# Kernel optimization log

Measured on AMD Instinct MI355X. Metric: run time of the kernel, lower is better.

Reference implementation:

```python
import jax, jax.numpy as jnp
from jax import lax
import numpy as np


def setup_inputs() -> dict:
    key = jax.random.key(0)
    ks = jax.random.split(key, 7)
    B, T, I, H, O = 8192, 512, 7, 7, 1
    s = 1.0 / np.sqrt(H)
    return {
        "x": jax.random.normal(ks[0], (B, T, I), dtype=jnp.float32),
        "W_ih": jax.random.normal(ks[1], (H, I), dtype=jnp.float32) * s,
        "W_hh": jax.random.normal(ks[2], (H, H), dtype=jnp.float32) * s,
        "b_ih": jax.random.normal(ks[3], (H,), dtype=jnp.float32) * s,
        "b_hh": jax.random.normal(ks[4], (H,), dtype=jnp.float32) * s,
        "W_fc": jax.random.normal(ks[5], (O, H), dtype=jnp.float32) * s,
        "b_fc": jax.random.normal(ks[6], (O,), dtype=jnp.float32) * s,
    }


def reference(x, W_ih, W_hh, b_ih, b_hh, W_fc, b_fc):
    # Vanilla tanh RNN: h_t = tanh(x_t W_ih^T + b_ih + h_{t-1} W_hh^T + b_hh)
    B, T, _ = x.shape
    H = W_hh.shape[0]
    # Precompute the input projection for all timesteps (one big GEMM).
    xp = jnp.einsum("bti,hi->bth", x, W_ih) + (b_ih + b_hh)  # [B,T,H]
    h0 = jnp.zeros((B, H), dtype=x.dtype)

    def step(h, xt):
        h = jnp.tanh(xt + h @ W_hh.T)
        return h, h

    hT, hs = lax.scan(step, h0, jnp.swapaxes(xp, 0, 1))  # hs: [T,B,H]
    out_seq = jnp.swapaxes(hs, 0, 1)  # [B,T,H]
    out = (jnp.einsum("bth,oh->bto", out_seq, W_fc) + b_fc).squeeze(-1)  # [B,T]
    hidden = hT[None]  # [1,B,H] matching torch's (num_layers, B, H)
    return (out, hidden)
```

## Files before the change

kernel.cpp:

```cpp
#include <hip/hip_runtime.h>
#include <stdint.h>


#define B_TOTAL 8192
#define T_STEPS 512

__device__ __forceinline__ float tanh_fast(float a) {
    float e = __builtin_amdgcn_exp2f(a * 2.8853900817779268f);
    float r = __builtin_amdgcn_rcpf(e + 1.0f);
    return __builtin_fmaf(-2.0f, r, 1.0f);
}

__global__ __launch_bounds__(256, 1) void rnn_kernel(
    const float* __restrict__ x,
    const float* __restrict__ Wih,
    const float* __restrict__ Whh,
    const float* __restrict__ bih,
    const float* __restrict__ bhh,
    const float* __restrict__ Wfc,
    const float* __restrict__ bfc,
    float* __restrict__ out)
{
    const int tid  = threadIdx.x;
    const int k    = tid & 7;
    const int b    = blockIdx.x * 32 + (tid >> 3);
    const int base = (tid & 63) & ~7;

    float wih[7], whh[7];
    float bias = 0.0f;
    if (k < 7) {
        #pragma unroll
        for (int i = 0; i < 7; ++i) {
            wih[i] = Wih[k * 7 + i];
            whh[i] = Whh[k * 7 + i];
        }
        bias = bih[k] + bhh[k];
    } else {
        #pragma unroll
        for (int i = 0; i < 7; ++i) { wih[i] = 0.0f; whh[i] = 0.0f; }
    }
    float wfc[7];
    #pragma unroll
    for (int j = 0; j < 7; ++j) wfc[j] = Wfc[j];
    const float bfcv = bfc[0];

    const float4* xrow = (const float4*)(x + (size_t)b * (T_STEPS * 7));

    float h[7];
    #pragma unroll
    for (int j = 0; j < 7; ++j) h[j] = 0.0f;

    float* outp = out + (size_t)b * T_STEPS;

    float4 bufA[14], bufB[14];
    #pragma unroll
    for (int i = 0; i < 14; ++i) bufA[i] = xrow[i];

    auto process = [&](const float4 (&buf)[14], int c) {
        float xv[56];
        #pragma unroll
        for (int i = 0; i < 14; ++i) {
            xv[4 * i + 0] = buf[i].x; xv[4 * i + 1] = buf[i].y;
            xv[4 * i + 2] = buf[i].z; xv[4 * i + 3] = buf[i].w;
        }
        float u[8];
        #pragma unroll
        for (int s = 0; s < 8; ++s) {
            float m0 = wih[0] * xv[s * 7 + 0];
            float m1 = wih[1] * xv[s * 7 + 1];
            float m2 = wih[2] * xv[s * 7 + 2];
            float m3 = wih[3] * xv[s * 7 + 3];
            float m4 = wih[4] * xv[s * 7 + 4];
            float m5 = wih[5] * xv[s * 7 + 5];
            float m6 = wih[6] * xv[s * 7 + 6];
            u[s] = ((m0 + m1) + (m2 + m3)) + ((m4 + m5) + (m6 + bias));
        }
        float o[8];
        #pragma unroll
        for (int s = 0; s < 8; ++s) {
            float r0 = whh[0] * h[0];
            float r1 = whh[1] * h[1];
            float r2 = whh[2] * h[2];
            float r3 = whh[3] * h[3];
            float r4 = whh[4] * h[4];
            float r5 = whh[5] * h[5];
            float r6 = whh[6] * h[6];
            float acc = u[s] + (((r0 + r1) + (r2 + r3)) + ((r4 + r5) + r6));
            float hk = tanh_fast(acc);
            #pragma unroll
            for (int j = 0; j < 7; ++j)
                h[j] = __shfl(hk, base + j, 64);
            float f0 = wfc[0] * h[0];
            float f1 = wfc[1] * h[1];
            float f2 = wfc[2] * h[2];
            float f3 = wfc[3] * h[3];
            float f4 = wfc[4] * h[4];
            float f5 = wfc[5] * h[5];
            float f6 = wfc[6] * h[6];
            o[s] = ((f0 + f1) + (f2 + f3)) + ((f4 + f5) + (f6 + bfcv));
        }
        if (k == 7) {
            float4 lo = make_float4(o[0], o[1], o[2], o[3]);
            float4 hi = make_float4(o[4], o[5], o[6], o[7]);
            *(float4*)(outp + c * 8 + 0) = lo;
            *(float4*)(outp + c * 8 + 4) = hi;
        }
    };

    for (int c = 0; c < 64; c += 2) {
        #pragma unroll
        for (int i = 0; i < 14; ++i) bufB[i] = xrow[(c + 1) * 14 + i];
        process(bufA, c);
        if (c + 2 < 64) {
            #pragma unroll
            for (int i = 0; i < 14; ++i) bufA[i] = xrow[(c + 2) * 14 + i];
        }
        process(bufB, c + 1);
    }

    if (k < 7) {
        out[(size_t)B_TOTAL * T_STEPS + (size_t)b * 7 + k] = h[k];
    }
}

extern "C" void kernel_launch(void* const* d_in, const int* in_sizes, int n_in,
                              void* d_out, int out_size, void* d_ws, size_t ws_size,
                              hipStream_t stream) {
    const float* x   = (const float*)d_in[0];
    const float* Wih = (const float*)d_in[1];
    const float* Whh = (const float*)d_in[2];
    const float* bih = (const float*)d_in[3];
    const float* bhh = (const float*)d_in[4];
    const float* Wfc = (const float*)d_in[5];
    const float* bfc = (const float*)d_in[6];
    float* out = (float*)d_out;

    rnn_kernel<<<dim3(B_TOTAL / 32), dim3(256), 0, stream>>>(
        x, Wih, Whh, bih, bhh, Wfc, bfc, out);
}
```

Before: 243.6 us.

## Replace LDS shuffles with DPP quad broadcasts for hidden-state exchange

Hidden-state exchange within each 8-lane group now uses DPP quad_perm broadcasts and a half-row mirror instead of seven __shfl (ds_bpermute) calls per timestep. Recurrent and output weights are pre-permuted per quad so each lane can consume its own quad's values and the mirrored values from the other quad. The dot products are also rewritten with explicit FMAs. This aims to shorten the serial per-step latency of the recurrence, at the cost of relying on exact DPP lane semantics.

```diff
diff --git a/kernel.cpp b/kernel.cpp
--- a/kernel.cpp
+++ b/kernel.cpp
@@ -4,6 +4,18 @@
 
 #define B_TOTAL 8192
 #define T_STEPS 512
+
+#define DPP_QUAD0 0x00
+#define DPP_QUAD1 0x55
+#define DPP_QUAD2 0xAA
+#define DPP_QUAD3 0xFF
+#define DPP_HALF_MIRROR 0x141
+
+template <int CTRL>
+__device__ __forceinline__ float dpp_mov(float v) {
+    int r = __builtin_amdgcn_update_dpp(0, __float_as_int(v), CTRL, 0xF, 0xF, true);
+    return __int_as_float(r);
+}
 
 __device__ __forceinline__ float tanh_fast(float a) {
     float e = __builtin_amdgcn_exp2f(a * 2.8853900817779268f);
@@ -24,33 +36,45 @@
     const int tid  = threadIdx.x;
     const int k    = tid & 7;
     const int b    = blockIdx.x * 32 + (tid >> 3);
-    const int base = (tid & 63) & ~7;
+    const int quad = (tid >> 2) & 1;
 
-    float wih[7], whh[7];
+    float wih[7];
+    float wa[4], wb[4], wfa[4], wfb[4];
     float bias = 0.0f;
-    if (k < 7) {
+    {
+        float whh_row[8];
         #pragma unroll
-        for (int i = 0; i < 7; ++i) {
-            wih[i] = Wih[k * 7 + i];
-            whh[i] = Whh[k * 7 + i];
+        for (int i = 0; i < 8; ++i) whh_row[i] = 0.0f;
+        if (k < 7) {
+            #pragma unroll
+            for (int i = 0; i < 7; ++i) {
+                wih[i] = Wih[k * 7 + i];
+                whh_row[i] = Whh[k * 7 + i];
+            }
+            bias = bih[k] + bhh[k];
+        } else {
+            #pragma unroll
+            for (int i = 0; i < 7; ++i) wih[i] = 0.0f;
         }
-        bias = bih[k] + bhh[k];
-    } else {
+        float wfc_row[8];
         #pragma unroll
-        for (int i = 0; i < 7; ++i) { wih[i] = 0.0f; whh[i] = 0.0f; }
+        for (int j = 0; j < 7; ++j) wfc_row[j] = Wfc[j];
+        wfc_row[7] = 0.0f;
+        #pragma unroll
+        for (int j = 0; j < 4; ++j) {
+            wa[j]  = quad ? whh_row[4 + j] : whh_row[j];
+            wb[j]  = quad ? whh_row[j]     : whh_row[4 + j];
+            wfa[j] = quad ? wfc_row[4 + j] : wfc_row[j];
+            wfb[j] = quad ? wfc_row[j]     : wfc_row[4 + j];
+        }
     }
-    float wfc[7];
-    #pragma unroll
-    for (int j = 0; j < 7; ++j) wfc[j] = Wfc[j];
     const float bfcv = bfc[0];
 
     const float4* xrow = (const float4*)(x + (size_t)b * (T_STEPS * 7));
+    float* outp = out + (size_t)b * T_STEPS;
 
-    float h[7];
-    #pragma unroll
-    for (int j = 0; j < 7; ++j) h[j] = 0.0f;
-
-    float* outp = out + (size_t)b * T_STEPS;
+    float a0 = 0.f, a1 = 0.f, a2 = 0.f, a3 = 0.f;
+    float b0 = 0.f, b1 = 0.f, b2 = 0.f, b3 = 0.f;
 
     float4 bufA[14], bufB[14];
     #pragma unroll
@@ -66,44 +90,40 @@
         float u[8];
         #pragma unroll
         for (int s = 0; s < 8; ++s) {
-            float m0 = wih[0] * xv[s * 7 + 0];
-            float m1 = wih[1] * xv[s * 7 + 1];
-            float m2 = wih[2] * xv[s * 7 + 2];
-            float m3 = wih[3] * xv[s * 7 + 3];
-            float m4 = wih[4] * xv[s * 7 + 4];
-            float m5 = wih[5] * xv[s * 7 + 5];
-            float m6 = wih[6] * xv[s * 7 + 6];
-            u[s] = ((m0 + m1) + (m2 + m3)) + ((m4 + m5) + (m6 + bias));
+            const float* xs = &xv[s * 7];
+            float p01 = __builtin_fmaf(wih[1], xs[1], wih[0] * xs[0]);
+            float p23 = __builtin_fmaf(wih[3], xs[3], wih[2] * xs[2]);
+            float p45 = __builtin_fmaf(wih[5], xs[5], wih[4] * xs[4]);
+            float p6b = __builtin_fmaf(wih[6], xs[6], bias);
+            u[s] = (p01 + p23) + (p45 + p6b);
         }
         float o[8];
         #pragma unroll
         for (int s = 0; s < 8; ++s) {
-            float r0 = whh[0] * h[0];
-            float r1 = whh[1] * h[1];
-            float r2 = whh[2] * h[2];
-            float r3 = whh[3] * h[3];
-            float r4 = whh[4] * h[4];
-            float r5 = whh[5] * h[5];
-            float r6 = whh[6] * h[6];
-            float acc = u[s] + (((r0 + r1) + (r2 + r3)) + ((r4 + r5) + r6));
+            float p0 = __builtin_fmaf(wa[0], a0, u[s]);
+            float p1 = __builtin_fmaf(wa[2], a2, wa[1] * a1);
+            float p2 = __builtin_fmaf(wb[0], b0, wa[3] * a3);
+            float p3 = __builtin_fmaf(wb[2], b2, wb[1] * b1);
+            float p4 = wb[3] * b3;
+            float acc = (p0 + p1) + (p2 + (p3 + p4));
             float hk = tanh_fast(acc);
-            #pragma unroll
-            for (int j = 0; j < 7; ++j)
-                h[j] = __shfl(hk, base + j, 64);
-            float f0 = wfc[0] * h[0];
-            float f1 = wfc[1] * h[1];
-            float f2 = wfc[2] * h[2];
-            float f3 = wfc[3] * h[3];
-            float f4 = wfc[4] * h[4];
-            float f5 = wfc[5] * h[5];
-            float f6 = wfc[6] * h[6];
-            o[s] = ((f0 + f1) + (f2 + f3)) + ((f4 + f5) + (f6 + bfcv));
+            a0 = dpp_mov<DPP_QUAD0>(hk);
+            a1 = dpp_mov<DPP_QUAD1>(hk);
+            a2 = dpp_mov<DPP_QUAD2>(hk);
+            a3 = dpp_mov<DPP_QUAD3>(hk);
+            b0 = dpp_mov<DPP_HALF_MIRROR>(a0);
+            b1 = dpp_mov<DPP_HALF_MIRROR>(a1);
+            b2 = dpp_mov<DPP_HALF_MIRROR>(a2);
+            b3 = dpp_mov<DPP_HALF_MIRROR>(a3);
+            float r0 = __builtin_fmaf(wfa[0], a0, bfcv);
+            float r1 = __builtin_fmaf(wfa[2], a2, wfa[1] * a1);
+            float r2 = __builtin_fmaf(wfb[1], b1, wfb[0] * b0);
+            float r3 = __builtin_fmaf(wfb[3], b3, wfb[2] * b2);
+            o[s] = (r0 + r1) + (r2 + r3);
         }
         if (k == 7) {
-            float4 lo = make_float4(o[0], o[1], o[2], o[3]);
-            float4 hi = make_float4(o[4], o[5], o[6], o[7]);
-            *(float4*)(outp + c * 8 + 0) = lo;
-            *(float4*)(outp + c * 8 + 4) = hi;
+            *(float4*)(outp + c * 8 + 0) = make_float4(o[0], o[1], o[2], o[3]);
+            *(float4*)(outp + c * 8 + 4) = make_float4(o[4], o[5], o[6], o[7]);
         }
     };
 
@@ -119,7 +139,9 @@
     }
 
     if (k < 7) {
-        out[(size_t)B_TOTAL * T_STEPS + (size_t)b * 7 + k] = h[k];
+        int kk = k & 3;
+        float hv = (kk == 0) ? a0 : (kk == 1) ? a1 : (kk == 2) ? a2 : a3;
+        out[(size_t)B_TOTAL * T_STEPS + (size_t)b * 7 + k] = hv;
     }
 }
 
```

Measured after the change: 224.2 us. 1.09x faster.
